# Optimization experiments

Hardware: AMD Instinct MI355X
Metric: run time of the kernel (lower is better)

Reference implementation:

```python
import jax, jax.numpy as jnp
import numpy as np

N_NODES = 100000
N_EDGES = 1700000  # 1.6M random edges + 100k self-loops (dgl.add_self_loop)
HID = 128
N_GRAPHS = 64
N_CLASSES = 10
T_STEPS = 5


def setup_inputs() -> dict:
    key = jax.random.key(0)
    ks = jax.random.split(key, 12)
    m = jax.random.normal(ks[0], (N_NODES,), dtype=jnp.float32)
    n_rand = N_EDGES - N_NODES
    src_r = jax.random.randint(ks[1], (n_rand,), 0, N_NODES)
    dst_r = jax.random.randint(ks[2], (n_rand,), 0, N_NODES)
    loops = jnp.arange(N_NODES)
    src = jnp.concatenate([src_r, loops])
    dst = jnp.concatenate([dst_r, loops])
    graph_ids = jnp.sort(jax.random.randint(ks[3], (N_NODES,), 0, N_GRAPHS))
    s = 0.05
    W_e = jax.random.normal(ks[4], (HID, HID), dtype=jnp.float32) * s
    b_e = jnp.zeros((HID,), dtype=jnp.float32)
    W_ih = jax.random.normal(ks[5], (3 * HID, HID), dtype=jnp.float32) * s
    b_ih = jnp.zeros((3 * HID,), dtype=jnp.float32)
    W_hh = jax.random.normal(ks[6], (3 * HID, HID), dtype=jnp.float32) * s
    b_hh = jnp.zeros((3 * HID,), dtype=jnp.float32)
    W_cls = jax.random.normal(ks[7], (N_CLASSES, HID), dtype=jnp.float32) * s
    b_cls = jnp.zeros((N_CLASSES,), dtype=jnp.float32)
    return {"m": m, "W_e": W_e, "b_e": b_e, "W_ih": W_ih, "b_ih": b_ih,
            "W_hh": W_hh, "b_hh": b_hh, "W_cls": W_cls, "b_cls": b_cls,
            "src": src, "dst": dst, "graph_ids": graph_ids, "n_graphs": N_GRAPHS}


def _gated_graph_forward(m, W_e, b_e, W_ih, b_ih, W_hh, b_hh, W_cls, b_cls,
                         src, dst, graph_ids, n_graphs):
    n_nodes = m.shape[0]
    hid = W_e.shape[0]
    # h = ndata['m'].view(-1,1), zero-padded to out_feats (DGL GatedGraphConv)
    h = jnp.zeros((n_nodes, hid), dtype=m.dtype).at[:, 0].set(m)
    for _ in range(T_STEPS):
        # single edge type: a[v] = sum_{(u,v) in E} W_e h[u] + b_e
        msg = (h @ W_e.T + b_e)[src]                       # [E, H]
        a = jax.ops.segment_sum(msg, dst, num_segments=n_nodes)
        # torch.nn.GRUCell(a, h); gate order: r, z, n
        gi = a @ W_ih.T + b_ih
        gh = h @ W_hh.T + b_hh
        i_r, i_z, i_n = jnp.split(gi, 3, axis=-1)
        h_r, h_z, h_n = jnp.split(gh, 3, axis=-1)
        r = jax.nn.sigmoid(i_r + h_r)
        z = jax.nn.sigmoid(i_z + h_z)
        n = jnp.tanh(i_n + r * h_n)
        h = (1.0 - z) * n + z * h
    h = jax.nn.relu(h)
    # dgl.mean_nodes: per-graph mean over nodes
    sums = jax.ops.segment_sum(h, graph_ids, num_segments=n_graphs)
    cnt = jax.ops.segment_sum(jnp.ones((n_nodes,), h.dtype), graph_ids,
                              num_segments=n_graphs)
    hg = sums / jnp.maximum(cnt, 1.0)[:, None]             # [G, H]
    return hg @ W_cls.T + b_cls                            # [G, C]


def reference(m, W_e, b_e, W_ih, b_ih, W_hh, b_hh, W_cls, b_cls,
              src, dst, graph_ids, n_graphs):
    return _gated_graph_forward(m, W_e, b_e, W_ih, b_ih, W_hh, b_hh,
                                W_cls, b_cls, src, dst, graph_ids, n_graphs)
```

## Files before the change

kernel.cpp:

```cpp
#include <hip/hip_runtime.h>

#define HID 128
#define G3  384
#define TSTEPS 5
#define BSHIFT 9
#define BNODES (1 << BSHIFT)
#define MAXBUK 256
#define PART_EPB 8192

typedef unsigned int  uint;
typedef unsigned short ushort;

typedef float  f32x4  __attribute__((ext_vector_type(4)));
typedef __bf16 bf16x8 __attribute__((ext_vector_type(8)));

union B8u { uint4 u; bf16x8 b; ushort s[8]; };

static __device__ inline ushort f2bf(float f) {
  uint u = __float_as_uint(f);
  uint r = u + 0x7fffu + ((u >> 16) & 1u);
  return (ushort)(r >> 16);
}
static __device__ inline float bf2f(ushort s) {
  return __uint_as_float(((uint)s) << 16);
}

__global__ __launch_bounds__(128) void k_weights(
    const float* __restrict__ W_e, const float* __restrict__ b_e,
    const float* __restrict__ W_ih, const float* __restrict__ W_hh,
    ushort* __restrict__ Wcomb, ushort* __restrict__ Whh16, float* __restrict__ bvec,
    ushort* __restrict__ Wc0, ushort* __restrict__ Wh0)
{
  int j = blockIdx.x, t = threadIdx.x;
  if (j < G3) {
    __shared__ float row[HID];
    row[t] = W_ih[j * HID + t];
    __syncthreads();
    float acc = 0.f;
    for (int k = 0; k < HID; ++k) acc = fmaf(row[k], W_e[k * HID + t], acc);
    Wcomb[j * HID + t] = f2bf(acc);
    if (t == 0) {
      Wc0[j] = f2bf(acc);
      float b = 0.f;
      for (int k = 0; k < HID; ++k) b += row[k] * b_e[k];
      bvec[j] = b;
    }
  } else {
    int j2 = j - G3;
    Whh16[j2 * HID + t] = f2bf(W_hh[j2 * HID + t]);
    if (t == 0) Wh0[j2] = f2bf(W_hh[j2 * HID]);
  }
}

__global__ __launch_bounds__(256) void k_bh(const int* __restrict__ dst,
                                            int* __restrict__ bhist, int E) {
  __shared__ int lh[MAXBUK];
  int t = threadIdx.x;
  if (t < MAXBUK) lh[t] = 0;
  __syncthreads();
  for (int e = blockIdx.x * 256 + t; e < E; e += gridDim.x * 256)
    atomicAdd(&lh[dst[e] >> BSHIFT], 1);
  __syncthreads();
  if (t < MAXBUK && lh[t]) atomicAdd(&bhist[t], lh[t]);
}

__global__ __launch_bounds__(256) void k_bsc(const int* __restrict__ bhist,
                                             int* __restrict__ bbase,
                                             int* __restrict__ gcur,
                                             int* __restrict__ rowptr, int E, int N) {
  __shared__ int ls[MAXBUK];
  int t = threadIdx.x;
  ls[t] = bhist[t];
  __syncthreads();
  if (t == 0) {
    int run = 0;
    for (int i = 0; i < MAXBUK; ++i) {
      bbase[i] = run; gcur[i] = run; run += ls[i];
    }
    bbase[MAXBUK] = run;
    rowptr[N] = E;
  }
}

__global__ __launch_bounds__(256) void k_part(
    const int* __restrict__ src, const int* __restrict__ dst,
    int* __restrict__ gcur, uint* __restrict__ ebuf, int E) {
  __shared__ int lh[MAXBUK], lbase[MAXBUK], lcur[MAXBUK];
  int t = threadIdx.x;
  int base = blockIdx.x * PART_EPB;
  if (t < MAXBUK) lh[t] = 0;
  __syncthreads();
#pragma unroll 4
  for (int j = 0; j < PART_EPB / 256; ++j) {
    int e = base + j * 256 + t;
    if (e < E) atomicAdd(&lh[dst[e] >> BSHIFT], 1);
  }
  __syncthreads();
  if (t < MAXBUK) {
    lbase[t] = lh[t] ? atomicAdd(&gcur[t], lh[t]) : 0;
    lcur[t] = 0;
  }
  __syncthreads();
#pragma unroll 4
  for (int j = 0; j < PART_EPB / 256; ++j) {
    int e = base + j * 256 + t;
    if (e < E) {
      int d = dst[e];
      int b = d >> BSHIFT;
      int p = atomicAdd(&lcur[b], 1);
      ebuf[lbase[b] + p] = (uint)src[e] | ((uint)(d & (BNODES - 1)) << 20);
    }
  }
}

__global__ __launch_bounds__(256) void k_fill2(
    const uint* __restrict__ ebuf, const int* __restrict__ bbase,
    int* __restrict__ csrc, int* __restrict__ rowptr, int* __restrict__ deg, int N) {
  __shared__ int hcnt[BNODES];
  __shared__ int wls[4];
  int t = threadIdx.x;
  int b = blockIdx.x;
  int ebeg = bbase[b], eend = bbase[b + 1];
  for (int i = t; i < BNODES; i += 256) hcnt[i] = 0;
  __syncthreads();
  for (int e = ebeg + t; e < eend; e += 256)
    atomicAdd(&hcnt[ebuf[e] >> 20], 1);
  __syncthreads();
  const int PER = BNODES / 256;
  int lane = t & 63, wv = t >> 6;
  int x[PER]; int s = 0;
#pragma unroll
  for (int i = 0; i < PER; ++i) { x[i] = hcnt[PER * t + i]; s += x[i]; }
  int incl = s;
#pragma unroll
  for (int off = 1; off < 64; off <<= 1) {
    int u = __shfl_up(incl, off, 64);
    if (lane >= off) incl += u;
  }
  if (lane == 63) wls[wv] = incl;
  __syncthreads();
  int wbase = 0;
  for (int i = 0; i < wv; ++i) wbase += wls[i];
  int run = wbase + incl - s;
#pragma unroll
  for (int i = 0; i < PER; ++i) {
    int node = (b << BSHIFT) + PER * t + i;
    hcnt[PER * t + i] = run;
    if (node < N) { rowptr[node] = ebeg + run; deg[node] = x[i]; }
    run += x[i];
  }
  __syncthreads();
  for (int e = ebeg + t; e < eend; e += 256) {
    uint v = ebuf[e];
    int p = atomicAdd(&hcnt[v >> 20], 1);
    csrc[ebeg + p] = (int)(v & 0xFFFFFu);
  }
}

__global__ void k_minit(const float* __restrict__ m, ushort* __restrict__ m16, int N) {
  int v = blockIdx.x * 256 + threadIdx.x;
  if (v < N) m16[v] = f2bf(m[v]);
}

__global__ __launch_bounds__(256) void k_gather0(
    const int* __restrict__ rowptr, const int* __restrict__ csrc,
    const ushort* __restrict__ m16, ushort* __restrict__ hsum0, int N)
{
  int v = blockIdx.x * 256 + threadIdx.x;
  if (v >= N) return;
  int beg = rowptr[v], end = rowptr[v + 1];
  float a0 = 0.f, a1 = 0.f, a2 = 0.f, a3 = 0.f;
  int e = beg;
  for (; e + 16 <= end; e += 16) {
    a0 += (bf2f(m16[csrc[e + 0]]) + bf2f(m16[csrc[e + 4]])) +
          (bf2f(m16[csrc[e + 8]]) + bf2f(m16[csrc[e + 12]]));
    a1 += (bf2f(m16[csrc[e + 1]]) + bf2f(m16[csrc[e + 5]])) +
          (bf2f(m16[csrc[e + 9]]) + bf2f(m16[csrc[e + 13]]));
    a2 += (bf2f(m16[csrc[e + 2]]) + bf2f(m16[csrc[e + 6]])) +
          (bf2f(m16[csrc[e + 10]]) + bf2f(m16[csrc[e + 14]]));
    a3 += (bf2f(m16[csrc[e + 3]]) + bf2f(m16[csrc[e + 7]])) +
          (bf2f(m16[csrc[e + 11]]) + bf2f(m16[csrc[e + 15]]));
  }
  for (; e < end; e += 4) {
    if (e + 0 < end) a0 += bf2f(m16[csrc[e + 0]]);
    if (e + 1 < end) a1 += bf2f(m16[csrc[e + 1]]);
    if (e + 2 < end) a2 += bf2f(m16[csrc[e + 2]]);
    if (e + 3 < end) a3 += bf2f(m16[csrc[e + 3]]);
  }
  hsum0[v] = f2bf((a0 + a1) + (a2 + a3));
}

__global__ __launch_bounds__(256) void k_gru0(
    const ushort* __restrict__ hsum0, const ushort* __restrict__ m16,
    const int* __restrict__ deg,
    const ushort* __restrict__ Wc0, const ushort* __restrict__ Wh0,
    const float* __restrict__ bvec, const float* __restrict__ b_ih,
    const float* __restrict__ b_hh, ushort* __restrict__ hbn, int N)
{
  int idx = blockIdx.x * 256 + threadIdx.x;
  if (idx >= N * HID) return;
  int n = idx >> 7, d = idx & (HID - 1);
  float s0 = bf2f(hsum0[n]);
  float h0 = bf2f(m16[n]);
  float degf = (float)deg[n];
  float acc0 = s0 * bf2f(Wc0[d]);
  float acc1 = s0 * bf2f(Wc0[d + 128]);
  float acc2 = s0 * bf2f(Wc0[d + 256]);
  float acc3 = h0 * bf2f(Wh0[d]);
  float acc4 = h0 * bf2f(Wh0[d + 128]);
  float acc5 = h0 * bf2f(Wh0[d + 256]);
  float hold = (d == 0) ? h0 : 0.f;
  float ir = acc0 + degf * bvec[d] + b_ih[d];
  float iz = acc1 + degf * bvec[d + 128] + b_ih[d + 128];
  float in_ = acc2 + degf * bvec[d + 256] + b_ih[d + 256];
  float hr = acc3 + b_hh[d];
  float hz = acc4 + b_hh[d + 128];
  float hn = acc5 + b_hh[d + 256];
  float r = __builtin_amdgcn_rcpf(1.f + __expf(-(ir + hr)));
  float z = __builtin_amdgcn_rcpf(1.f + __expf(-(iz + hz)));
  float x2 = in_ + r * hn;
  float e2 = __expf(2.f * x2);
  float nv = 1.f - 2.f * __builtin_amdgcn_rcpf(e2 + 1.f);
  float hv = (1.f - z) * nv + z * hold;
  hbn[idx] = f2bf(hv);
}

__global__ __launch_bounds__(256) void k_gather(
    const int* __restrict__ rowptr, const int* __restrict__ csrc,
    const ushort* __restrict__ hb, ushort* __restrict__ hs16, int N, int nstrip)
{
  int x = blockIdx.x & 7;
  int ii = blockIdx.x >> 3;
  int s = 8 * (ii >> 2) + x;
  if (s >= nstrip) return;
  int v = s * 16 + (ii & 3) * 4 + (threadIdx.x >> 6);
  if (v >= N) return;
  int lane = threadIdx.x & 63;
  int g = lane >> 4;
  int i = lane & 15;
  int beg = rowptr[v], end = rowptr[v + 1];
  float acc[8] = {0.f, 0.f, 0.f, 0.f, 0.f, 0.f, 0.f, 0.f};
  int e = beg;
  for (; e + 16 <= end; e += 16) {
    int s0 = csrc[e + g];
    int s1 = csrc[e + 4 + g];
    int s2 = csrc[e + 8 + g];
    int s3 = csrc[e + 12 + g];
    B8u w0; w0.u = *(const uint4*)(hb + (size_t)s0 * HID + i * 8);
    B8u w1; w1.u = *(const uint4*)(hb + (size_t)s1 * HID + i * 8);
    B8u w2; w2.u = *(const uint4*)(hb + (size_t)s2 * HID + i * 8);
    B8u w3; w3.u = *(const uint4*)(hb + (size_t)s3 * HID + i * 8);
#pragma unroll
    for (int j = 0; j < 8; ++j)
      acc[j] += (bf2f(w0.s[j]) + bf2f(w1.s[j])) + (bf2f(w2.s[j]) + bf2f(w3.s[j]));
  }
  for (; e < end; e += 4) {
    int ee = e + g;
    if (ee < end) {
      int s0 = csrc[ee];
      B8u w; w.u = *(const uint4*)(hb + (size_t)s0 * HID + i * 8);
#pragma unroll
      for (int j = 0; j < 8; ++j) acc[j] += bf2f(w.s[j]);
    }
  }
#pragma unroll
  for (int j = 0; j < 8; ++j) {
    acc[j] += __shfl_xor(acc[j], 16, 64);
    acc[j] += __shfl_xor(acc[j], 32, 64);
  }
  if (g == 0) {
    uint4 ov;
    ov.x = ((uint)f2bf(acc[1]) << 16) | (uint)f2bf(acc[0]);
    ov.y = ((uint)f2bf(acc[3]) << 16) | (uint)f2bf(acc[2]);
    ov.z = ((uint)f2bf(acc[5]) << 16) | (uint)f2bf(acc[4]);
    ov.w = ((uint)f2bf(acc[7]) << 16) | (uint)f2bf(acc[6]);
    *(uint4*)(hs16 + (size_t)v * HID + i * 8) = ov;
  }
}

struct GruCtx {
  const ushort* hs16; const ushort* hbc; ushort* hbn; const int* deg;
  int l16, quad, d;
  float bir, biz, bin_, bhr, bhz, bhn, vr, vz, vn;
};

static __device__ __forceinline__ void gru_load(
    const GruCtx& c, int s, B8u af[4], B8u hf[4], float hold[4], float degf[4]) {
  int n0 = s << 4;
  size_t arow = (size_t)(n0 + c.l16) * HID + c.quad * 8;
#pragma unroll
  for (int kc = 0; kc < 4; ++kc) {
    af[kc].u = *(const uint4*)(c.hs16 + arow + kc * 32);
    hf[kc].u = *(const uint4*)(c.hbc + arow + kc * 32);
  }
#pragma unroll
  for (int rg = 0; rg < 4; ++rg) {
    int n = n0 + c.quad * 4 + rg;
    hold[rg] = bf2f(c.hbc[(size_t)n * HID + c.d]);
    degf[rg] = (float)c.deg[n];
  }
}

static __device__ __forceinline__ void gru_compute(
    const GruCtx& c, int s, const B8u af[4], const B8u hf[4],
    const float hold[4], const float degf[4],
    const B8u bw[3][4], const B8u bh[3][4]) {
  f32x4 acc[6] = {};
#pragma unroll
  for (int kc = 0; kc < 4; ++kc)
#pragma unroll
    for (int g = 0; g < 3; ++g) {
      acc[g]     = __builtin_amdgcn_mfma_f32_16x16x32_bf16(af[kc].b, bw[g][kc].b, acc[g], 0, 0, 0);
      acc[3 + g] = __builtin_amdgcn_mfma_f32_16x16x32_bf16(hf[kc].b, bh[g][kc].b, acc[3 + g], 0, 0, 0);
    }
  int n0 = s << 4;
#pragma unroll
  for (int rg = 0; rg < 4; ++rg) {
    float ir = acc[0][rg] + degf[rg] * c.vr + c.bir;
    float iz = acc[1][rg] + degf[rg] * c.vz + c.biz;
    float in_ = acc[2][rg] + degf[rg] * c.vn + c.bin_;
    float hr = acc[3][rg] + c.bhr;
    float hz = acc[4][rg] + c.bhz;
    float hn = acc[5][rg] + c.bhn;
    float r = __builtin_amdgcn_rcpf(1.f + __expf(-(ir + hr)));
    float z = __builtin_amdgcn_rcpf(1.f + __expf(-(iz + hz)));
    float x2 = in_ + r * hn;
    float e2 = __expf(2.f * x2);
    float nv = 1.f - 2.f * __builtin_amdgcn_rcpf(e2 + 1.f);
    float hv = (1.f - z) * nv + z * hold[rg];
    c.hbn[(size_t)(n0 + c.quad * 4 + rg) * HID + c.d] = f2bf(hv);
  }
}

__global__ __launch_bounds__(512, 2) void k_gru(
    const ushort* __restrict__ hs16,
    const ushort* __restrict__ hbc, ushort* __restrict__ hbn,
    const ushort* __restrict__ Wcomb, const ushort* __restrict__ Whh16,
    const float* __restrict__ bvec, const float* __restrict__ b_ih,
    const float* __restrict__ b_hh, const int* __restrict__ deg, int N)
{
  const int w = threadIdx.x >> 6;
  const int lane = threadIdx.x & 63;
  const int quad = lane >> 4, l16 = lane & 15;
  const int d0 = w * 16;
  const int d = d0 + l16;

  B8u bw[3][4], bh[3][4];
#pragma unroll
  for (int g = 0; g < 3; ++g)
#pragma unroll
    for (int kc = 0; kc < 4; ++kc) {
      int j = (d0 + g * 128 + l16) * HID + kc * 32 + quad * 8;
      bw[g][kc].u = *(const uint4*)(Wcomb + j);
      bh[g][kc].u = *(const uint4*)(Whh16 + j);
    }

  GruCtx c;
  c.hs16 = hs16; c.hbc = hbc; c.hbn = hbn; c.deg = deg;
  c.l16 = l16; c.quad = quad; c.d = d;
  c.bir = b_ih[d]; c.biz = b_ih[d + 128]; c.bin_ = b_ih[d + 256];
  c.bhr = b_hh[d]; c.bhz = b_hh[d + 128]; c.bhn = b_hh[d + 256];
  c.vr = bvec[d]; c.vz = bvec[d + 128]; c.vn = bvec[d + 256];

  const int nstrip = N >> 4;
  const int G = (int)gridDim.x;
  int s = blockIdx.x;
  if (s >= nstrip) return;

  B8u afA[4], hfA[4], afB[4], hfB[4];
  float holdA[4], degA[4], holdB[4], degB[4];
  gru_load(c, s, afA, hfA, holdA, degA);

  while (true) {
    int ns = s + G;
    bool more = ns < nstrip;
    if (more) gru_load(c, ns, afB, hfB, holdB, degB);
    gru_compute(c, s, afA, hfA, holdA, degA, bw, bh);
    if (!more) break;
    s = ns;
    ns = s + G;
    more = ns < nstrip;
    if (more) gru_load(c, ns, afA, hfA, holdA, degA);
    gru_compute(c, s, afB, hfB, holdB, degB, bw, bh);
    if (!more) break;
    s = ns;
  }
}

__global__ __launch_bounds__(64) void k_bounds(const int* __restrict__ gid,
                                               int* __restrict__ cnt, int N, int G) {
  int g = threadIdx.x;
  if (g >= G) return;
  int lo = 0, hi = N;
  while (lo < hi) { int mid = (lo + hi) >> 1; if (gid[mid] < g) lo = mid + 1; else hi = mid; }
  int lb0 = lo;
  lo = 0; hi = N;
  int g1 = g + 1;
  while (lo < hi) { int mid = (lo + hi) >> 1; if (gid[mid] < g1) lo = mid + 1; else hi = mid; }
  cnt[g] = lo - lb0;
}

#define POOL_CHUNK 96
__global__ __launch_bounds__(128) void k_pool(const ushort* __restrict__ hb,
                                              const int* __restrict__ gid,
                                              float* __restrict__ hg, int N) {
  int d = threadIdx.x;
  int start = blockIdx.x * POOL_CHUNK;
  if (start >= N) return;
  int end = min(start + POOL_CHUNK, N);
  float acc = 0.f;
  int g = gid[start];
  for (int n = start; n < end; ++n) {
    int gn = gid[n];
    if (gn != g) { unsafeAtomicAdd(&hg[g * HID + d], acc); acc = 0.f; g = gn; }
    acc += fmaxf(bf2f(hb[(size_t)n * HID + d]), 0.f);
  }
  unsafeAtomicAdd(&hg[g * HID + d], acc);
}

__global__ __launch_bounds__(640) void k_cls(const float* __restrict__ hg,
                                             const int* __restrict__ cnt,
                                             const float* __restrict__ Wc,
                                             const float* __restrict__ bc,
                                             float* __restrict__ out, int G) {
  int t = threadIdx.x;
  if (t >= G * 10) return;
  int g = t / 10, c = t % 10;
  float inv = 1.f / fmaxf((float)cnt[g], 1.f);
  float acc = 0.f;
  for (int d = 0; d < HID; ++d) acc = fmaf(hg[g * HID + d], Wc[c * HID + d], acc);
  out[t] = acc * inv + bc[c];
}

extern "C" void kernel_launch(void* const* d_in, const int* in_sizes, int n_in,
                              void* d_out, int out_size, void* d_ws, size_t ws_size,
                              hipStream_t stream) {
  const int N = in_sizes[0];
  const int E = in_sizes[9];
  const float* m    = (const float*)d_in[0];
  const float* W_e  = (const float*)d_in[1];
  const float* b_e  = (const float*)d_in[2];
  const float* W_ih = (const float*)d_in[3];
  const float* b_ih = (const float*)d_in[4];
  const float* W_hh = (const float*)d_in[5];
  const float* b_hh = (const float*)d_in[6];
  const float* W_cls = (const float*)d_in[7];
  const float* b_cls = (const float*)d_in[8];
  const int* src = (const int*)d_in[9];
  const int* dst = (const int*)d_in[10];
  const int* gid = (const int*)d_in[11];
  const int G = out_size / 10;
  float* out = (float*)d_out;

  size_t off = 0;
  auto alloc = [&](size_t b) {
    char* p = (char*)d_ws + off;
    off += (b + 255) & ~(size_t)255;
    return (void*)p;
  };
  ushort* hb0    = (ushort*)alloc((size_t)N * HID * 2);
  ushort* hb1    = (ushort*)alloc((size_t)N * HID * 2);
  ushort* hs16   = (ushort*)alloc((size_t)N * HID * 2);
  int*    deg    = (int*)   alloc((size_t)N * 4);
  int*    rowptr = (int*)   alloc((size_t)(N + 1) * 4);
  int*    csrc   = (int*)   alloc((size_t)E * 4);
  uint*   ebuf   = (uint*)  alloc((size_t)E * 4);
  int*    bhist  = (int*)   alloc((size_t)MAXBUK * 4);
  int*    bbase  = (int*)   alloc((size_t)(MAXBUK + 1) * 4);
  int*    gcur   = (int*)   alloc((size_t)MAXBUK * 4);
  ushort* Wcomb  = (ushort*)alloc((size_t)G3 * HID * 2);
  ushort* Whh16  = (ushort*)alloc((size_t)G3 * HID * 2);
  float*  bvec   = (float*) alloc((size_t)G3 * 4);
  float*  hg     = (float*) alloc((size_t)G * HID * 4);
  int*    cnt    = (int*)   alloc((size_t)G * 4);
  ushort* m16    = (ushort*)alloc((size_t)N * 2);
  ushort* hsum0  = (ushort*)alloc((size_t)N * 2);
  ushort* Wc0    = (ushort*)alloc((size_t)G3 * 2);
  ushort* Wh0    = (ushort*)alloc((size_t)G3 * 2);
  if (off > ws_size) return;

  const int NBUK = (N + BNODES - 1) >> BSHIFT;

  k_weights<<<2 * G3, HID, 0, stream>>>(W_e, b_e, W_ih, W_hh, Wcomb, Whh16, bvec, Wc0, Wh0);
  k_minit<<<(N + 255) / 256, 256, 0, stream>>>(m, m16, N);
  hipMemsetAsync(bhist, 0, (size_t)MAXBUK * 4, stream);
  k_bh<<<256, 256, 0, stream>>>(dst, bhist, E);
  k_bsc<<<1, MAXBUK, 0, stream>>>(bhist, bbase, gcur, rowptr, E, N);
  k_part<<<(E + PART_EPB - 1) / PART_EPB, 256, 0, stream>>>(src, dst, gcur, ebuf, E);
  k_fill2<<<NBUK, 256, 0, stream>>>(ebuf, bbase, csrc, rowptr, deg, N);

  k_gather0<<<(N + 255) / 256, 256, 0, stream>>>(rowptr, csrc, m16, hsum0, N);
  k_gru0<<<(N * HID + 255) / 256, 256, 0, stream>>>(hsum0, m16, deg, Wc0, Wh0,
                                                    bvec, b_ih, b_hh, hb1, N);

  ushort* hbc = hb1;
  ushort* hbn = hb0;
  const int nstrip = N >> 4;
  const int gather_blocks = 8 * ((nstrip + 7) / 8) * 4;
  const int gru_blocks = nstrip < 1024 ? nstrip : 1024;
  for (int s = 1; s < TSTEPS; ++s) {
    k_gather<<<gather_blocks, 256, 0, stream>>>(rowptr, csrc, hbc, hs16, N, nstrip);
    k_gru<<<gru_blocks, 512, 0, stream>>>(hs16, hbc, hbn, Wcomb, Whh16, bvec, b_ih, b_hh, deg, N);
    ushort* t = hbc; hbc = hbn; hbn = t;
  }

  hipMemsetAsync(hg, 0, (size_t)G * HID * 4, stream);
  k_bounds<<<1, 64, 0, stream>>>(gid, cnt, N, G);
  k_pool<<<(N + POOL_CHUNK - 1) / POOL_CHUNK, HID, 0, stream>>>(hbc, gid, hg, N);
  k_cls<<<1, 640, 0, stream>>>(hg, cnt, W_cls, b_cls, out, G);
}
```

Baseline: 826.4 us.

## Split GRU input and hidden matmuls across wave groups with LDS exchange

The GRU kernel now uses 1024-thread blocks. Half the waves compute the input-side gate matmul and the other half the hidden-side matmul, so each wave holds only one set of weight fragments in registers. Partial results pass through a shared-memory tile and the gate epilogue is recomputed in a coalesced row/column layout. This cuts per-thread register pressure and allows higher occupancy. In exchange it adds two block-wide barriers per strip and LDS traffic, and cuts the grid to 256 blocks.

```diff
diff --git a/kernel.cpp b/kernel.cpp
--- a/kernel.cpp
+++ b/kernel.cpp
@@ -278,110 +278,124 @@
   }
 }
 
-struct GruCtx {
-  const ushort* hs16; const ushort* hbc; ushort* hbn; const int* deg;
-  int l16, quad, d;
+struct GruCtx2 {
+  const ushort* Amat;
+  const ushort* hbc; ushort* hbn; const int* deg;
+  int l16, quad, gm3, d0, ecol, erow0;
   float bir, biz, bin_, bhr, bhz, bhn, vr, vz, vn;
 };
 
-static __device__ __forceinline__ void gru_load(
-    const GruCtx& c, int s, B8u af[4], B8u hf[4], float hold[4], float degf[4]) {
+static __device__ __forceinline__ void gru2_loadA(const GruCtx2& c, int s, B8u a[4]) {
+  size_t arow = (size_t)(s * 16 + c.l16) * HID + c.quad * 8;
+#pragma unroll
+  for (int kc = 0; kc < 4; ++kc)
+    a[kc].u = *(const uint4*)(c.Amat + arow + kc * 32);
+}
+
+static __device__ __forceinline__ void gru2_loadE(const GruCtx2& c, int s,
+                                                  float hold[2], float dg[2]) {
   int n0 = s << 4;
-  size_t arow = (size_t)(n0 + c.l16) * HID + c.quad * 8;
-#pragma unroll
-  for (int kc = 0; kc < 4; ++kc) {
-    af[kc].u = *(const uint4*)(c.hs16 + arow + kc * 32);
-    hf[kc].u = *(const uint4*)(c.hbc + arow + kc * 32);
-  }
-#pragma unroll
-  for (int rg = 0; rg < 4; ++rg) {
-    int n = n0 + c.quad * 4 + rg;
-    hold[rg] = bf2f(c.hbc[(size_t)n * HID + c.d]);
-    degf[rg] = (float)c.deg[n];
-  }
-}
-
-static __device__ __forceinline__ void gru_compute(
-    const GruCtx& c, int s, const B8u af[4], const B8u hf[4],
-    const float hold[4], const float degf[4],
-    const B8u bw[3][4], const B8u bh[3][4]) {
-  f32x4 acc[6] = {};
+  hold[0] = bf2f(c.hbc[(size_t)(n0 + c.erow0) * HID + c.ecol]);
+  hold[1] = bf2f(c.hbc[(size_t)(n0 + c.erow0 + 8) * HID + c.ecol]);
+  dg[0] = (float)c.deg[n0 + c.erow0];
+  dg[1] = (float)c.deg[n0 + c.erow0 + 8];
+}
+
+static __device__ __forceinline__ void gru2_step(
+    const GruCtx2& c, int s, const B8u a[4], const float hold[2], const float dg[2],
+    const B8u bfr[3][4], float (*S)[16][132]) {
+  f32x4 acc[3] = {};
 #pragma unroll
   for (int kc = 0; kc < 4; ++kc)
 #pragma unroll
-    for (int g = 0; g < 3; ++g) {
-      acc[g]     = __builtin_amdgcn_mfma_f32_16x16x32_bf16(af[kc].b, bw[g][kc].b, acc[g], 0, 0, 0);
-      acc[3 + g] = __builtin_amdgcn_mfma_f32_16x16x32_bf16(hf[kc].b, bh[g][kc].b, acc[3 + g], 0, 0, 0);
-    }
+    for (int g = 0; g < 3; ++g)
+      acc[g] = __builtin_amdgcn_mfma_f32_16x16x32_bf16(a[kc].b, bfr[g][kc].b, acc[g], 0, 0, 0);
+  __builtin_amdgcn_s_barrier();
+#pragma unroll
+  for (int g = 0; g < 3; ++g)
+#pragma unroll
+    for (int rg = 0; rg < 4; ++rg)
+      S[c.gm3 + g][c.quad * 4 + rg][c.d0 + c.l16] = acc[g][rg];
+  asm volatile("s_waitcnt lgkmcnt(0)" ::: "memory");
+  __builtin_amdgcn_sched_barrier(0);
+  __builtin_amdgcn_s_barrier();
   int n0 = s << 4;
 #pragma unroll
-  for (int rg = 0; rg < 4; ++rg) {
-    float ir = acc[0][rg] + degf[rg] * c.vr + c.bir;
-    float iz = acc[1][rg] + degf[rg] * c.vz + c.biz;
-    float in_ = acc[2][rg] + degf[rg] * c.vn + c.bin_;
-    float hr = acc[3][rg] + c.bhr;
-    float hz = acc[4][rg] + c.bhz;
-    float hn = acc[5][rg] + c.bhn;
+  for (int k = 0; k < 2; ++k) {
+    int row = c.erow0 + 8 * k;
+    float ir  = S[0][row][c.ecol] + dg[k] * c.vr + c.bir;
+    float iz  = S[1][row][c.ecol] + dg[k] * c.vz + c.biz;
+    float in_ = S[2][row][c.ecol] + dg[k] * c.vn + c.bin_;
+    float hr  = S[3][row][c.ecol] + c.bhr;
+    float hz  = S[4][row][c.ecol] + c.bhz;
+    float hn  = S[5][row][c.ecol] + c.bhn;
     float r = __builtin_amdgcn_rcpf(1.f + __expf(-(ir + hr)));
     float z = __builtin_amdgcn_rcpf(1.f + __expf(-(iz + hz)));
     float x2 = in_ + r * hn;
     float e2 = __expf(2.f * x2);
     float nv = 1.f - 2.f * __builtin_amdgcn_rcpf(e2 + 1.f);
-    float hv = (1.f - z) * nv + z * hold[rg];
-    c.hbn[(size_t)(n0 + c.quad * 4 + rg) * HID + c.d] = f2bf(hv);
-  }
-}
-
-__global__ __launch_bounds__(512, 2) void k_gru(
+    float hv = (1.f - z) * nv + z * hold[k];
+    c.hbn[(size_t)(n0 + row) * HID + c.ecol] = f2bf(hv);
+  }
+}
+
+__global__ __launch_bounds__(1024, 4) void k_gru(
     const ushort* __restrict__ hs16,
     const ushort* __restrict__ hbc, ushort* __restrict__ hbn,
     const ushort* __restrict__ Wcomb, const ushort* __restrict__ Whh16,
     const float* __restrict__ bvec, const float* __restrict__ b_ih,
     const float* __restrict__ b_hh, const int* __restrict__ deg, int N)
 {
-  const int w = threadIdx.x >> 6;
-  const int lane = threadIdx.x & 63;
+  __shared__ float S[6][16][132];
+  const int tid = threadIdx.x;
+  const int w = tid >> 6;
+  const int lane = tid & 63;
   const int quad = lane >> 4, l16 = lane & 15;
-  const int d0 = w * 16;
-  const int d = d0 + l16;
-
-  B8u bw[3][4], bh[3][4];
+  const int gm = w >> 3;
+  const int gw = w & 7;
+  const int d0 = gw * 16;
+
+  const ushort* Wmat = gm ? Whh16 : Wcomb;
+
+  B8u bfr[3][4];
 #pragma unroll
   for (int g = 0; g < 3; ++g)
 #pragma unroll
     for (int kc = 0; kc < 4; ++kc) {
       int j = (d0 + g * 128 + l16) * HID + kc * 32 + quad * 8;
-      bw[g][kc].u = *(const uint4*)(Wcomb + j);
-      bh[g][kc].u = *(const uint4*)(Whh16 + j);
+      bfr[g][kc].u = *(const uint4*)(Wmat + j);
     }
 
-  GruCtx c;
-  c.hs16 = hs16; c.hbc = hbc; c.hbn = hbn; c.deg = deg;
-  c.l16 = l16; c.quad = quad; c.d = d;
-  c.bir = b_ih[d]; c.biz = b_ih[d + 128]; c.bin_ = b_ih[d + 256];
-  c.bhr = b_hh[d]; c.bhz = b_hh[d + 128]; c.bhn = b_hh[d + 256];
-  c.vr = bvec[d]; c.vz = bvec[d + 128]; c.vn = bvec[d + 256];
+  GruCtx2 c;
+  c.Amat = gm ? hbc : hs16;
+  c.hbc = hbc; c.hbn = hbn; c.deg = deg;
+  c.l16 = l16; c.quad = quad; c.gm3 = gm * 3; c.d0 = d0;
+  c.ecol = tid & 127;
+  c.erow0 = tid >> 7;
+  c.bir = b_ih[c.ecol]; c.biz = b_ih[c.ecol + 128]; c.bin_ = b_ih[c.ecol + 256];
+  c.bhr = b_hh[c.ecol]; c.bhz = b_hh[c.ecol + 128]; c.bhn = b_hh[c.ecol + 256];
+  c.vr = bvec[c.ecol]; c.vz = bvec[c.ecol + 128]; c.vn = bvec[c.ecol + 256];
 
   const int nstrip = N >> 4;
   const int G = (int)gridDim.x;
   int s = blockIdx.x;
   if (s >= nstrip) return;
 
-  B8u afA[4], hfA[4], afB[4], hfB[4];
-  float holdA[4], degA[4], holdB[4], degB[4];
-  gru_load(c, s, afA, hfA, holdA, degA);
+  B8u aA[4], aB[4];
+  float hA[2], dA[2], hB[2], dB[2];
+  gru2_loadA(c, s, aA); gru2_loadE(c, s, hA, dA);
 
   while (true) {
     int ns = s + G;
     bool more = ns < nstrip;
-    if (more) gru_load(c, ns, afB, hfB, holdB, degB);
-    gru_compute(c, s, afA, hfA, holdA, degA, bw, bh);
+    if (more) { gru2_loadA(c, ns, aB); gru2_loadE(c, ns, hB, dB); }
+    gru2_step(c, s, aA, hA, dA, bfr, S);
     if (!more) break;
     s = ns;
     ns = s + G;
     more = ns < nstrip;
-    if (more) gru_load(c, ns, afA, hfA, holdA, degA);
-    gru_compute(c, s, afB, hfB, holdB, degB, bw, bh);
+    if (more) { gru2_loadA(c, ns, aA); gru2_loadE(c, ns, hA, dA); }
+    gru2_step(c, s, aB, hB, dB, bfr, S);
     if (!more) break;
     s = ns;
   }
@@ -497,10 +511,10 @@
   ushort* hbn = hb0;
   const int nstrip = N >> 4;
   const int gather_blocks = 8 * ((nstrip + 7) / 8) * 4;
-  const int gru_blocks = nstrip < 1024 ? nstrip : 1024;
+  const int gru_blocks = nstrip < 256 ? nstrip : 256;
   for (int s = 1; s < TSTEPS; ++s) {
     k_gather<<<gather_blocks, 256, 0, stream>>>(rowptr, csrc, hbc, hs16, N, nstrip);
-    k_gru<<<gru_blocks, 512, 0, stream>>>(hs16, hbc, hbn, Wcomb, Whh16, bvec, b_ih, b_hh, deg, N);
+    k_gru<<<gru_blocks, 1024, 0, stream>>>(hs16, hbc, hbn, Wcomb, Whh16, bvec, b_ih, b_hh, deg, N);
     ushort* t = hbc; hbc = hbn; hbn = t;
   }
 
```

Result: no change. 812.0 us (-1.7%).
